# Kernel optimization log

Measured on AMD Instinct MI355X. Metric: run time of the kernel, lower is better.

## Reference

```python
import jax, jax.numpy as jnp
import numpy as np

B, H, W, C = 4, 64, 64, 128
NH, K = 4, 7
HD = C // NH
MLPD = 4 * C
EPS = 1e-5

def _ln(x, g, b):
    m = x.mean(-1, keepdims=True)
    v = ((x - m) ** 2).mean(-1, keepdims=True)
    return (x - m) * jax.lax.rsqrt(v + EPS) * g + b

def setup_inputs() -> dict:
    key = jax.random.key(0)
    ks = jax.random.split(key, 10)
    rn = lambda k, s: jax.random.normal(k, s, dtype=jnp.float32) * 0.02
    return {
        'query': jax.random.normal(ks[0], (B, H, W, C), dtype=jnp.float32),
        'key_value': jax.random.normal(ks[1], (B, H, W, C), dtype=jnp.float32),
        'g1': jnp.ones((C,), jnp.float32), 'b1': jnp.zeros((C,), jnp.float32),
        'g2': jnp.ones((C,), jnp.float32), 'b2': jnp.zeros((C,), jnp.float32),
        'g3': jnp.ones((C,), jnp.float32), 'b3': jnp.zeros((C,), jnp.float32),
        'Wq': rn(ks[2], (C, C)), 'bq': jnp.zeros((C,), jnp.float32),
        'Wkv': rn(ks[3], (C, 2 * C)), 'bkv': jnp.zeros((2 * C,), jnp.float32),
        'Wp': rn(ks[4], (C, C)), 'bp': jnp.zeros((C,), jnp.float32),
        'rpb': rn(ks[5], (NH, 2 * K - 1, 2 * K - 1)),
        'W1': rn(ks[6], (C, MLPD)), 'bm1': jnp.zeros((MLPD,), jnp.float32),
        'W2': rn(ks[7], (MLPD, C)), 'bm2': jnp.zeros((C,), jnp.float32),
    }

def _nat(qn, kvn, Wq, bq, Wkv, bkv, Wp, bp, rpb):
    # NATTEN-style 2D neighborhood attention (clamped KxK window at borders)
    q = (qn @ Wq + bq).reshape(B, H, W, NH, HD) * (HD ** -0.5)
    kv = (kvn @ Wkv + bkv).reshape(B, H, W, 2, NH, HD)
    k, v = kv[..., 0, :, :], kv[..., 1, :, :]
    ii = jnp.clip(jnp.arange(H) - K // 2, 0, H - K)[:, None] + jnp.arange(K)  # [H,K]
    jj = jnp.clip(jnp.arange(W) - K // 2, 0, W - K)[:, None] + jnp.arange(K)  # [W,K]
    def gather(t):  # [B,H,W,NH,HD] -> [B,H,W,NH,K*K,HD]
        t = jnp.take(t, ii, axis=1)   # [B,H,K,W,NH,HD]
        t = jnp.take(t, jj, axis=3)   # [B,H,K,W,K,NH,HD]
        return t.transpose(0, 1, 3, 5, 2, 4, 6).reshape(B, H, W, NH, K * K, HD)
    kn, vn = gather(k), gather(v)
    scores = jnp.einsum('bijhd,bijhnd->bijhn', q, kn)  # [B,H,W,NH,K*K]
    # relative positional bias: offsets in [-(K-1), K-1] -> index into 2K-1 table
    ri = ii - jnp.arange(H)[:, None] + (K - 1)  # [H,K]
    rj = jj - jnp.arange(W)[:, None] + (K - 1)  # [W,K]
    bias = rpb[:, ri]                   # [NH,H,K,2K-1]
    bias = jnp.take(bias, rj, axis=3)   # [NH,H,K,W,K]
    bias = bias.transpose(1, 3, 0, 2, 4).reshape(H, W, NH, K * K)
    attn = jax.nn.softmax(scores + bias[None], axis=-1)
    out = jnp.einsum('bijhn,bijhnd->bijhd', attn, vn).reshape(B, H, W, C)
    return out @ Wp + bp

def reference(query, key_value, g1, b1, g2, b2, g3, b3, Wq, bq, Wkv, bkv, Wp, bp, rpb, W1, bm1, W2, bm2):
    shortcut = key_value
    qn = _ln(query, g1, b1)
    kvn = _ln(key_value, g2, b2)
    x = shortcut + _nat(qn, kvn, Wq, bq, Wkv, bkv, Wp, bp, rpb)
    h = _ln(x, g3, b3)
    h = jax.nn.gelu(h @ W1 + bm1, approximate=False) @ W2 + bm2
    return x + h
```

## Files before the change

kernel.cpp:

```cpp
#include <hip/hip_runtime.h>
#include <math.h>

#define TOK 16384

typedef __attribute__((ext_vector_type(8))) __bf16 bf16x8;
typedef __attribute__((ext_vector_type(4))) float f32x4;

__device__ inline unsigned short f2bf(float f) {
    union { float f; unsigned int u; } v; v.f = f;
    unsigned int r = v.u + 0x7fffu + ((v.u >> 16) & 1u);
    return (unsigned short)(r >> 16);
}

__device__ inline void ln_body(const float* __restrict__ x, const float* __restrict__ g,
                               const float* __restrict__ b, unsigned short* __restrict__ y,
                               int tok, int lane)
{
    float2 v = ((const float2*)(x + (size_t)tok * 128))[lane];
    float s = v.x + v.y;
#pragma unroll
    for (int m = 32; m >= 1; m >>= 1) s += __shfl_xor(s, m);
    float mean = s * (1.0f / 128.0f);
    float dx = v.x - mean, dy = v.y - mean;
    float vs = dx * dx + dy * dy;
#pragma unroll
    for (int m = 32; m >= 1; m >>= 1) vs += __shfl_xor(vs, m);
    float rs = rsqrtf(vs * (1.0f / 128.0f) + 1e-5f);
    float2 gg = ((const float2*)g)[lane];
    float2 bb = ((const float2*)b)[lane];
    float ox = dx * rs * gg.x + bb.x;
    float oy = dy * rs * gg.y + bb.y;
    unsigned int pk = (unsigned int)f2bf(ox) | ((unsigned int)f2bf(oy) << 16);
    ((unsigned int*)(y + (size_t)tok * 128))[lane] = pk;
}

__global__ __launch_bounds__(256) void prep_kernel(
    const float* __restrict__ query, const float* __restrict__ key_value,
    const float* __restrict__ g1, const float* __restrict__ b1,
    const float* __restrict__ g2, const float* __restrict__ b2,
    const float* __restrict__ Wq, const float* __restrict__ Wkv,
    const float* __restrict__ Wp, const float* __restrict__ W1, const float* __restrict__ W2,
    unsigned short* __restrict__ qnh, unsigned short* __restrict__ kvnh,
    unsigned short* __restrict__ Wt)
{
    int blk = blockIdx.x, tid = threadIdx.x;
    if (blk < 8192) {
        int lane = tid & 63;
        if (blk < 4096) ln_body(query,     g1, b1, qnh,  blk * 4 + (tid >> 6), lane);
        else            ln_body(key_value, g2, b2, kvnh, (blk - 4096) * 4 + (tid >> 6), lane);
        return;
    }
    __shared__ float tile[32][33];
    int t = blk - 8192;
    const float* src; unsigned short* dst; int Kd, Nd, li;
    if      (t < 16)  { src = Wq;  dst = Wt;          Kd = 128; Nd = 128; li = t; }
    else if (t < 48)  { src = Wkv; dst = Wt + 16384;  Kd = 128; Nd = 256; li = t - 16; }
    else if (t < 64)  { src = Wp;  dst = Wt + 49152;  Kd = 128; Nd = 128; li = t - 48; }
    else if (t < 128) { src = W1;  dst = Wt + 65536;  Kd = 128; Nd = 512; li = t - 64; }
    else              { src = W2;  dst = Wt + 131072; Kd = 512; Nd = 128; li = t - 128; }
    int ntc = Nd >> 5;
    int k0 = (li / ntc) * 32, n0 = (li % ntc) * 32;
    int r = tid >> 3, c4 = (tid & 7) * 4;
    float4 v = *(const float4*)(src + (size_t)(k0 + r) * Nd + n0 + c4);
    tile[r][c4 + 0] = v.x; tile[r][c4 + 1] = v.y;
    tile[r][c4 + 2] = v.z; tile[r][c4 + 3] = v.w;
    __syncthreads();
    ushort4 o;
    o.x = f2bf(tile[c4 + 0][r]);
    o.y = f2bf(tile[c4 + 1][r]);
    o.z = f2bf(tile[c4 + 2][r]);
    o.w = f2bf(tile[c4 + 3][r]);
    *(ushort4*)(dst + (size_t)(n0 + r) * Kd + k0 + c4) = o;
}

template<int MODE, int TK>
__global__ __launch_bounds__(256) void gemm_mfma(
    const unsigned short* __restrict__ A, const unsigned short* __restrict__ Wt,
    const float* __restrict__ bias, const float* __restrict__ res,
    float* __restrict__ outF, unsigned short* __restrict__ outH,
    unsigned short* __restrict__ vtg, int N, float scale)
{
    const int wave = threadIdx.x >> 6, lane = threadIdx.x & 63;
    const int wm = wave & 1, wn = wave >> 1;
    const int m0 = blockIdx.x * 64 + wm * 32;
    const int n0 = blockIdx.y * 64 + wn * 32;
    const int lr = lane & 15, lg = lane >> 4;
    f32x4 acc[2][2] = {};
#pragma unroll 8
    for (int k0 = 0; k0 < TK; k0 += 32) {
        bf16x8 a[2], b[2];
#pragma unroll
        for (int mf = 0; mf < 2; ++mf)
            a[mf] = *(const bf16x8*)(A + (size_t)(m0 + mf * 16 + lr) * TK + k0 + lg * 8);
#pragma unroll
        for (int nf = 0; nf < 2; ++nf)
            b[nf] = *(const bf16x8*)(Wt + (size_t)(n0 + nf * 16 + lr) * TK + k0 + lg * 8);
#pragma unroll
        for (int mf = 0; mf < 2; ++mf)
#pragma unroll
            for (int nf = 0; nf < 2; ++nf)
                acc[mf][nf] = __builtin_amdgcn_mfma_f32_16x16x32_bf16(a[mf], b[nf], acc[mf][nf], 0, 0, 0);
    }
#pragma unroll
    for (int nf = 0; nf < 2; ++nf) {
        int gc = n0 + nf * 16 + lr;
        float bs = bias[gc];
        if (MODE == 3 && gc >= 128) {
            int d = gc - 128;
            int hh = d >> 5, dd = d & 31;
#pragma unroll
            for (int mf = 0; mf < 2; ++mf) {
                int gr0 = m0 + mf * 16 + lg * 4;
                int bidx = gr0 >> 12, pos = gr0 & 4095;
                ushort4 pk;
                pk.x = f2bf(acc[mf][nf][0] + bs);
                pk.y = f2bf(acc[mf][nf][1] + bs);
                pk.z = f2bf(acc[mf][nf][2] + bs);
                pk.w = f2bf(acc[mf][nf][3] + bs);
                *(ushort4*)(vtg + ((size_t)((bidx * 4 + hh) * 32 + dd)) * 4096 + pos) = pk;
            }
            continue;
        }
#pragma unroll
        for (int mf = 0; mf < 2; ++mf) {
            int gr0 = m0 + mf * 16 + lg * 4;
#pragma unroll
            for (int r = 0; r < 4; ++r) {
                float v = acc[mf][nf][r] + bs;
                if (MODE == 0) outH[(size_t)(gr0 + r) * N + gc] = f2bf(v * scale);
                if (MODE == 1) { size_t idx = (size_t)(gr0 + r) * N + gc; outF[idx] = v + res[idx]; }
                if (MODE == 2) {
                    float gl = 0.5f * v * (1.0f + erff(v * 0.70710678118654752f));
                    outH[(size_t)(gr0 + r) * N + gc] = f2bf(gl);
                }
                if (MODE == 3) outH[(size_t)(gr0 + r) * 128 + gc] = f2bf(v);
            }
        }
    }
}

__global__ __launch_bounds__(256) void gemm_p_ln(
    const unsigned short* __restrict__ A, const unsigned short* __restrict__ Wt,
    const float* __restrict__ bias, const float* __restrict__ res,
    const float* __restrict__ g, const float* __restrict__ bln,
    float* __restrict__ xb, unsigned short* __restrict__ y)
{
    __shared__ float xs[32][132];
    const int wave = threadIdx.x >> 6, lane = threadIdx.x & 63;
    const int m0 = blockIdx.x * 32;
    const int n0 = wave * 32;
    const int lr = lane & 15, lg = lane >> 4;
    f32x4 acc[2][2] = {};
#pragma unroll
    for (int k0 = 0; k0 < 128; k0 += 32) {
        bf16x8 a[2], b[2];
#pragma unroll
        for (int mf = 0; mf < 2; ++mf)
            a[mf] = *(const bf16x8*)(A + (size_t)(m0 + mf * 16 + lr) * 128 + k0 + lg * 8);
#pragma unroll
        for (int nf = 0; nf < 2; ++nf)
            b[nf] = *(const bf16x8*)(Wt + (size_t)(n0 + nf * 16 + lr) * 128 + k0 + lg * 8);
#pragma unroll
        for (int mf = 0; mf < 2; ++mf)
#pragma unroll
            for (int nf = 0; nf < 2; ++nf)
                acc[mf][nf] = __builtin_amdgcn_mfma_f32_16x16x32_bf16(a[mf], b[nf], acc[mf][nf], 0, 0, 0);
    }
#pragma unroll
    for (int nf = 0; nf < 2; ++nf) {
        int gc = n0 + nf * 16 + lr;
        float bs = bias[gc];
#pragma unroll
        for (int mf = 0; mf < 2; ++mf) {
            int lr0 = mf * 16 + lg * 4;
#pragma unroll
            for (int r = 0; r < 4; ++r) {
                size_t idx = (size_t)(m0 + lr0 + r) * 128 + gc;
                float v = acc[mf][nf][r] + bs + res[idx];
                xb[idx] = v;
                xs[lr0 + r][gc] = v;
            }
        }
    }
    __syncthreads();
    const int r = threadIdx.x >> 3, t8 = threadIdx.x & 7;
    float vals[16];
#pragma unroll
    for (int j = 0; j < 16; ++j) vals[j] = xs[r][t8 * 16 + j];
    float s = 0.0f;
#pragma unroll
    for (int j = 0; j < 16; ++j) s += vals[j];
    s += __shfl_xor(s, 1); s += __shfl_xor(s, 2); s += __shfl_xor(s, 4);
    float mean = s * (1.0f / 128.0f);
    float vv = 0.0f;
#pragma unroll
    for (int j = 0; j < 16; ++j) { float d = vals[j] - mean; vv += d * d; }
    vv += __shfl_xor(vv, 1); vv += __shfl_xor(vv, 2); vv += __shfl_xor(vv, 4);
    float rs = rsqrtf(vv * (1.0f / 128.0f) + 1e-5f);
#pragma unroll
    for (int jj = 0; jj < 4; ++jj) {
        float4 gg = ((const float4*)g)[t8 * 4 + jj];
        float4 bb = ((const float4*)bln)[t8 * 4 + jj];
        ushort4 o;
        o.x = f2bf((vals[jj * 4 + 0] - mean) * rs * gg.x + bb.x);
        o.y = f2bf((vals[jj * 4 + 1] - mean) * rs * gg.y + bb.y);
        o.z = f2bf((vals[jj * 4 + 2] - mean) * rs * gg.z + bb.z);
        o.w = f2bf((vals[jj * 4 + 3] - mean) * rs * gg.w + bb.w);
        *(ushort4*)(y + (size_t)(m0 + r) * 128 + t8 * 16 + jj * 4) = o;
    }
}

__global__ __launch_bounds__(256) void nat_attn(
    const unsigned short* __restrict__ qbh,
    const unsigned short* __restrict__ kbh,
    const unsigned short* __restrict__ vtg,
    const float* __restrict__ rpb,
    unsigned short* __restrict__ out)
{
    __shared__ __align__(16) unsigned short Pbuf[4][16][232];
    __shared__ float rpbs[169];
    const int tid = threadIdx.x;
    const int wave = tid >> 6, lane = tid & 63;
    const int c = lane & 15, lg = lane >> 4;
    const int bid = blockIdx.x;
    const int tile = bid & 63, h = (bid >> 6) & 3, b = bid >> 8;
    const int ti0 = (tile >> 3) * 8, tj0 = (tile & 7) * 8;
    const int hr0 = min(max(ti0 - 3, 0), 50);
    const int hc0 = min(max(tj0 - 3, 0), 50);
    const int bb = b << 12;
    if (tid < 169) rpbs[tid] = rpb[h * 169 + tid];
    __syncthreads();

    const int gi_m = ti0 + wave * 2 + (c >> 3);
    const int gj_m = tj0 + (c & 7);
    const int tq = bb + gi_m * 64 + gj_m;
    bf16x8 qf = *(const bf16x8*)(qbh + (size_t)tq * 128 + h * 32 + lg * 8);

    bf16x8 kf[14];
    const int tk0 = bb + hr0 * 64 + hc0 + c;
#pragma unroll
    for (int kb = 0; kb < 14; ++kb)
        kf[kb] = *(const bf16x8*)(kbh + (size_t)(tk0 + kb * 64) * 128 + h * 32 + lg * 8);

    f32x4 S[14];
#pragma unroll
    for (int kb = 0; kb < 14; ++kb) {
        f32x4 z = {0.0f, 0.0f, 0.0f, 0.0f};
        S[kb] = __builtin_amdgcn_mfma_f32_16x16x32_bf16(qf, kf[kb], z, 0, 0, 0);
    }

    bf16x8 vf[7][2];
    const size_t vbase = (size_t)((b * 4 + h) * 32) * 4096;
#pragma unroll
    for (int ks = 0; ks < 7; ++ks) {
        int p0 = ks * 32 + lg * 8;
        size_t posa = (size_t)(hr0 + (p0 >> 4)) * 64 + hc0 + (p0 & 15);
#pragma unroll
        for (int nb = 0; nb < 2; ++nb)
            vf[ks][nb] = *(const bf16x8*)(vtg + vbase + (size_t)(nb * 16 + c) * 4096 + posa);
    }

#pragma unroll
    for (int i = 0; i < 4; ++i) {
        int m = lg * 4 + i;
        int gi = ti0 + wave * 2 + (m >> 3);
        int gj = tj0 + (m & 7);
        int si = min(max(gi - 3, 0), 57), sj = min(max(gj - 3, 0), 57);
        bool cv = (unsigned)(hc0 + c - sj) < 7u;
        int rjc = min(max(hc0 + c - gj + 6, 0), 12);
        float mxi = -INFINITY;
#pragma unroll
        for (int kb = 0; kb < 14; ++kb) {
            bool rv = (unsigned)(hr0 + kb - si) < 7u;
            int ric = min(max(hr0 + kb - gi + 6, 0), 12);
            float bias = rpbs[rjc + ric * 13];
            float s = (rv && cv) ? S[kb][i] + bias : -1e30f;
            S[kb][i] = s;
            mxi = fmaxf(mxi, s);
        }
        mxi = fmaxf(mxi, __shfl_xor(mxi, 1));
        mxi = fmaxf(mxi, __shfl_xor(mxi, 2));
        mxi = fmaxf(mxi, __shfl_xor(mxi, 4));
        mxi = fmaxf(mxi, __shfl_xor(mxi, 8));
        float smi = 0.0f;
#pragma unroll
        for (int kb = 0; kb < 14; ++kb) {
            float e = expf(S[kb][i] - mxi);
            S[kb][i] = e;
            smi += e;
        }
        smi += __shfl_xor(smi, 1);
        smi += __shfl_xor(smi, 2);
        smi += __shfl_xor(smi, 4);
        smi += __shfl_xor(smi, 8);
        float rinv = 1.0f / smi;
#pragma unroll
        for (int kb = 0; kb < 14; ++kb)
            Pbuf[wave][m][kb * 16 + c] = f2bf(S[kb][i] * rinv);
    }

    f32x4 O[2] = {};
#pragma unroll
    for (int ks = 0; ks < 7; ++ks) {
        bf16x8 pf = *(const bf16x8*)&Pbuf[wave][c][ks * 32 + lg * 8];
#pragma unroll
        for (int nb = 0; nb < 2; ++nb)
            O[nb] = __builtin_amdgcn_mfma_f32_16x16x32_bf16(pf, vf[ks][nb], O[nb], 0, 0, 0);
    }
#pragma unroll
    for (int i = 0; i < 4; ++i) {
        int m = lg * 4 + i;
        int gi = ti0 + wave * 2 + (m >> 3);
        int gj = tj0 + (m & 7);
        size_t t = ((size_t)(bb + gi * 64 + gj)) * 128 + h * 32;
        out[t + c]      = f2bf(O[0][i]);
        out[t + 16 + c] = f2bf(O[1][i]);
    }
}

extern "C" void kernel_launch(void* const* d_in, const int* in_sizes, int n_in,
                              void* d_out, int out_size, void* d_ws, size_t ws_size,
                              hipStream_t stream) {
    const float* query     = (const float*)d_in[0];
    const float* key_value = (const float*)d_in[1];
    const float* g1 = (const float*)d_in[2];
    const float* b1 = (const float*)d_in[3];
    const float* g2 = (const float*)d_in[4];
    const float* b2 = (const float*)d_in[5];
    const float* g3 = (const float*)d_in[6];
    const float* b3 = (const float*)d_in[7];
    const float* Wq  = (const float*)d_in[8];
    const float* bq  = (const float*)d_in[9];
    const float* Wkv = (const float*)d_in[10];
    const float* bkv = (const float*)d_in[11];
    const float* Wp  = (const float*)d_in[12];
    const float* bp  = (const float*)d_in[13];
    const float* rpb = (const float*)d_in[14];
    const float* W1  = (const float*)d_in[15];
    const float* bm1 = (const float*)d_in[16];
    const float* W2  = (const float*)d_in[17];
    const float* bm2 = (const float*)d_in[18];

    char* ws = (char*)d_ws;
    float*          xb   = (float*)(ws + 0);
    unsigned short* bufD = (unsigned short*)(ws + 8388608);
    unsigned short* kvnh = (unsigned short*)(ws + 12582912);
    unsigned short* qbh  = (unsigned short*)(ws + 16777216);
    unsigned short* kbh  = (unsigned short*)(ws + 20971520);
    unsigned short* vtg  = (unsigned short*)(ws + 25165824);
    unsigned short* h1h  = (unsigned short*)(ws + 29360128);
    unsigned short* Wt   = (unsigned short*)(ws + 46137344);
    unsigned short* WtQ  = Wt;
    unsigned short* WtKV = Wt + 16384;
    unsigned short* WtP  = Wt + 49152;
    unsigned short* WtW1 = Wt + 65536;
    unsigned short* WtW2 = Wt + 131072;

    const float qscale = 0.17677669529663687f;

    prep_kernel<<<8384, 256, 0, stream>>>(query, key_value, g1, b1, g2, b2,
                                          Wq, Wkv, Wp, W1, W2, bufD, kvnh, Wt);
    gemm_mfma<0,128><<<dim3(256, 2), 256, 0, stream>>>(bufD, WtQ,  bq,  nullptr, nullptr, qbh, nullptr, 128, qscale);
    gemm_mfma<3,128><<<dim3(256, 4), 256, 0, stream>>>(kvnh, WtKV, bkv, nullptr, nullptr, kbh, vtg,     256, 1.0f);
    nat_attn<<<1024, 256, 0, stream>>>(qbh, kbh, vtg, rpb, bufD);
    gemm_p_ln<<<512, 256, 0, stream>>>(bufD, WtP, bp, key_value, g3, b3, xb, kvnh);
    gemm_mfma<2,128><<<dim3(256, 8), 256, 0, stream>>>(kvnh, WtW1, bm1, nullptr, nullptr, h1h, nullptr, 512, 1.0f);
    gemm_mfma<1,512><<<dim3(256, 2), 256, 0, stream>>>(h1h,  WtW2, bm2, xb, (float*)d_out, nullptr, nullptr, 128, 1.0f);
}
```

Before: 206.3 us.

## Merge Q/KV GEMMs, use single-wave GEMM tiles, stage K/V in LDS for attention

Replaces the separate Q and KV projection launches with one gemm_qkv launch. The GEMMs now use 64-thread single-wave blocks, each computing a 32x64 tile. V is written token-major instead of as a transposed global layout, and nat_attn loads the 14x16 K/V halo once into shared memory, transposing V there, instead of each wave gathering K and V from global memory. This removes redundant global loads across the four waves and one launch, at the cost of more shared memory, extra barriers and possible LDS bank conflicts on the strided V transpose writes.

Result: faster. 181.9 us (-11.8%).

```diff
diff --git a/kernel.cpp b/kernel.cpp
--- a/kernel.cpp
+++ b/kernel.cpp
@@ -4,6 +4,7 @@
 #define TOK 16384
 
 typedef __attribute__((ext_vector_type(8))) __bf16 bf16x8;
+typedef __attribute__((ext_vector_type(4))) __bf16 bf16x4;
 typedef __attribute__((ext_vector_type(4))) float f32x4;
 
 __device__ inline unsigned short f2bf(float f) {
@@ -73,67 +74,100 @@
     *(ushort4*)(dst + (size_t)(n0 + r) * Kd + k0 + c4) = o;
 }
 
-template<int MODE, int TK>
-__global__ __launch_bounds__(256) void gemm_mfma(
-    const unsigned short* __restrict__ A, const unsigned short* __restrict__ Wt,
-    const float* __restrict__ bias, const float* __restrict__ res,
-    float* __restrict__ outF, unsigned short* __restrict__ outH,
-    unsigned short* __restrict__ vtg, int N, float scale)
-{
-    const int wave = threadIdx.x >> 6, lane = threadIdx.x & 63;
-    const int wm = wave & 1, wn = wave >> 1;
-    const int m0 = blockIdx.x * 64 + wm * 32;
-    const int n0 = blockIdx.y * 64 + wn * 32;
+__global__ __launch_bounds__(64) void gemm_qkv(
+    const unsigned short* __restrict__ qnh, const unsigned short* __restrict__ kvnh,
+    const unsigned short* __restrict__ Wt,
+    const float* __restrict__ bq, const float* __restrict__ bkv,
+    unsigned short* __restrict__ qbh, unsigned short* __restrict__ kbh,
+    unsigned short* __restrict__ vbh, float qscale)
+{
+    const int lane = threadIdx.x;
     const int lr = lane & 15, lg = lane >> 4;
-    f32x4 acc[2][2] = {};
-#pragma unroll 8
-    for (int k0 = 0; k0 < TK; k0 += 32) {
-        bf16x8 a[2], b[2];
-#pragma unroll
-        for (int mf = 0; mf < 2; ++mf)
-            a[mf] = *(const bf16x8*)(A + (size_t)(m0 + mf * 16 + lr) * TK + k0 + lg * 8);
-#pragma unroll
-        for (int nf = 0; nf < 2; ++nf)
-            b[nf] = *(const bf16x8*)(Wt + (size_t)(n0 + nf * 16 + lr) * TK + k0 + lg * 8);
-#pragma unroll
-        for (int mf = 0; mf < 2; ++mf)
-#pragma unroll
-            for (int nf = 0; nf < 2; ++nf)
+    const int y = blockIdx.y;
+    const unsigned short* A;
+    const unsigned short* Wb;
+    const float* bias;
+    int n0;
+    if (y < 2) { A = qnh;  Wb = Wt;          bias = bq;  n0 = y * 64; }
+    else       { A = kvnh; Wb = Wt + 16384;  bias = bkv; n0 = (y - 2) * 64; }
+    const int m0 = blockIdx.x * 32;
+    f32x4 acc[2][4] = {};
+#pragma unroll
+    for (int k0 = 0; k0 < 128; k0 += 32) {
+        bf16x8 a[2], b[4];
+#pragma unroll
+        for (int mf = 0; mf < 2; ++mf)
+            a[mf] = *(const bf16x8*)(A + (size_t)(m0 + mf * 16 + lr) * 128 + k0 + lg * 8);
+#pragma unroll
+        for (int nf = 0; nf < 4; ++nf)
+            b[nf] = *(const bf16x8*)(Wb + (size_t)(n0 + nf * 16 + lr) * 128 + k0 + lg * 8);
+#pragma unroll
+        for (int mf = 0; mf < 2; ++mf)
+#pragma unroll
+            for (int nf = 0; nf < 4; ++nf)
                 acc[mf][nf] = __builtin_amdgcn_mfma_f32_16x16x32_bf16(a[mf], b[nf], acc[mf][nf], 0, 0, 0);
     }
 #pragma unroll
-    for (int nf = 0; nf < 2; ++nf) {
+    for (int nf = 0; nf < 4; ++nf) {
         int gc = n0 + nf * 16 + lr;
         float bs = bias[gc];
-        if (MODE == 3 && gc >= 128) {
-            int d = gc - 128;
-            int hh = d >> 5, dd = d & 31;
-#pragma unroll
-            for (int mf = 0; mf < 2; ++mf) {
-                int gr0 = m0 + mf * 16 + lg * 4;
-                int bidx = gr0 >> 12, pos = gr0 & 4095;
-                ushort4 pk;
-                pk.x = f2bf(acc[mf][nf][0] + bs);
-                pk.y = f2bf(acc[mf][nf][1] + bs);
-                pk.z = f2bf(acc[mf][nf][2] + bs);
-                pk.w = f2bf(acc[mf][nf][3] + bs);
-                *(ushort4*)(vtg + ((size_t)((bidx * 4 + hh) * 32 + dd)) * 4096 + pos) = pk;
-            }
-            continue;
-        }
 #pragma unroll
         for (int mf = 0; mf < 2; ++mf) {
             int gr0 = m0 + mf * 16 + lg * 4;
 #pragma unroll
             for (int r = 0; r < 4; ++r) {
                 float v = acc[mf][nf][r] + bs;
-                if (MODE == 0) outH[(size_t)(gr0 + r) * N + gc] = f2bf(v * scale);
-                if (MODE == 1) { size_t idx = (size_t)(gr0 + r) * N + gc; outF[idx] = v + res[idx]; }
+                size_t tok = (size_t)(gr0 + r);
+                if (y < 2)          qbh[tok * 128 + gc] = f2bf(v * qscale);
+                else if (gc < 128)  kbh[tok * 128 + gc] = f2bf(v);
+                else                vbh[tok * 128 + gc - 128] = f2bf(v);
+            }
+        }
+    }
+}
+
+template<int MODE, int TK>
+__global__ __launch_bounds__(64) void gemm_w(
+    const unsigned short* __restrict__ A, const unsigned short* __restrict__ Wb,
+    const float* __restrict__ bias, const float* __restrict__ res,
+    float* __restrict__ outF, unsigned short* __restrict__ outH, int N)
+{
+    const int lane = threadIdx.x;
+    const int lr = lane & 15, lg = lane >> 4;
+    const int m0 = blockIdx.x * 32;
+    const int n0 = blockIdx.y * 64;
+    f32x4 acc[2][4] = {};
+#pragma unroll 4
+    for (int k0 = 0; k0 < TK; k0 += 32) {
+        bf16x8 a[2], b[4];
+#pragma unroll
+        for (int mf = 0; mf < 2; ++mf)
+            a[mf] = *(const bf16x8*)(A + (size_t)(m0 + mf * 16 + lr) * TK + k0 + lg * 8);
+#pragma unroll
+        for (int nf = 0; nf < 4; ++nf)
+            b[nf] = *(const bf16x8*)(Wb + (size_t)(n0 + nf * 16 + lr) * TK + k0 + lg * 8);
+#pragma unroll
+        for (int mf = 0; mf < 2; ++mf)
+#pragma unroll
+            for (int nf = 0; nf < 4; ++nf)
+                acc[mf][nf] = __builtin_amdgcn_mfma_f32_16x16x32_bf16(a[mf], b[nf], acc[mf][nf], 0, 0, 0);
+    }
+#pragma unroll
+    for (int nf = 0; nf < 4; ++nf) {
+        int gc = n0 + nf * 16 + lr;
+        float bs = bias[gc];
+#pragma unroll
+        for (int mf = 0; mf < 2; ++mf) {
+            int gr0 = m0 + mf * 16 + lg * 4;
+#pragma unroll
+            for (int r = 0; r < 4; ++r) {
+                float v = acc[mf][nf][r] + bs;
+                size_t idx = (size_t)(gr0 + r) * N + gc;
+                if (MODE == 1) outF[idx] = v + res[idx];
                 if (MODE == 2) {
                     float gl = 0.5f * v * (1.0f + erff(v * 0.70710678118654752f));
-                    outH[(size_t)(gr0 + r) * N + gc] = f2bf(gl);
+                    outH[idx] = f2bf(gl);
                 }
-                if (MODE == 3) outH[(size_t)(gr0 + r) * 128 + gc] = f2bf(v);
             }
         }
     }
@@ -213,11 +247,12 @@
 __global__ __launch_bounds__(256) void nat_attn(
     const unsigned short* __restrict__ qbh,
     const unsigned short* __restrict__ kbh,
-    const unsigned short* __restrict__ vtg,
+    const unsigned short* __restrict__ vbh,
     const float* __restrict__ rpb,
     unsigned short* __restrict__ out)
 {
-    __shared__ __align__(16) unsigned short Pbuf[4][16][232];
+    __shared__ unsigned short KP[14848];
+    __shared__ unsigned short Vsm[32 * 232];
     __shared__ float rpbs[169];
     const int tid = threadIdx.x;
     const int wave = tid >> 6, lane = tid & 63;
@@ -228,37 +263,36 @@
     const int hr0 = min(max(ti0 - 3, 0), 50);
     const int hc0 = min(max(tj0 - 3, 0), 50);
     const int bb = b << 12;
+
     if (tid < 169) rpbs[tid] = rpb[h * 169 + tid];
-    __syncthreads();
+
+    for (int u = tid; u < 896; u += 256) {
+        int tok = u >> 2, chunk = u & 3;
+        int tr = tok >> 4, tc = tok & 15;
+        size_t src = (size_t)(bb + (hr0 + tr) * 64 + hc0 + tc) * 128 + h * 32 + chunk * 8;
+        int4 kw = *(const int4*)(kbh + src);
+        *(int4*)&KP[tok * 40 + chunk * 8] = kw;
+        int4 vw = *(const int4*)(vbh + src);
+        const unsigned short* v8 = (const unsigned short*)&vw;
+#pragma unroll
+        for (int k = 0; k < 8; ++k)
+            Vsm[(chunk * 8 + k) * 232 + tok] = v8[k];
+    }
 
     const int gi_m = ti0 + wave * 2 + (c >> 3);
     const int gj_m = tj0 + (c & 7);
     const int tq = bb + gi_m * 64 + gj_m;
     bf16x8 qf = *(const bf16x8*)(qbh + (size_t)tq * 128 + h * 32 + lg * 8);
-
-    bf16x8 kf[14];
-    const int tk0 = bb + hr0 * 64 + hc0 + c;
-#pragma unroll
-    for (int kb = 0; kb < 14; ++kb)
-        kf[kb] = *(const bf16x8*)(kbh + (size_t)(tk0 + kb * 64) * 128 + h * 32 + lg * 8);
+    __syncthreads();
 
     f32x4 S[14];
 #pragma unroll
     for (int kb = 0; kb < 14; ++kb) {
+        bf16x8 kf = *(const bf16x8*)&KP[(kb * 16 + c) * 40 + lg * 8];
         f32x4 z = {0.0f, 0.0f, 0.0f, 0.0f};
-        S[kb] = __builtin_amdgcn_mfma_f32_16x16x32_bf16(qf, kf[kb], z, 0, 0, 0);
-    }
-
-    bf16x8 vf[7][2];
-    const size_t vbase = (size_t)((b * 4 + h) * 32) * 4096;
-#pragma unroll
-    for (int ks = 0; ks < 7; ++ks) {
-        int p0 = ks * 32 + lg * 8;
-        size_t posa = (size_t)(hr0 + (p0 >> 4)) * 64 + hc0 + (p0 & 15);
-#pragma unroll
-        for (int nb = 0; nb < 2; ++nb)
-            vf[ks][nb] = *(const bf16x8*)(vtg + vbase + (size_t)(nb * 16 + c) * 4096 + posa);
-    }
+        S[kb] = __builtin_amdgcn_mfma_f32_16x16x32_bf16(qf, kf, z, 0, 0, 0);
+    }
+    __syncthreads();
 
 #pragma unroll
     for (int i = 0; i < 4; ++i) {
@@ -296,16 +330,24 @@
         float rinv = 1.0f / smi;
 #pragma unroll
         for (int kb = 0; kb < 14; ++kb)
-            Pbuf[wave][m][kb * 16 + c] = f2bf(S[kb][i] * rinv);
+            KP[(wave * 16 + m) * 232 + kb * 16 + c] = f2bf(S[kb][i] * rinv);
     }
 
     f32x4 O[2] = {};
 #pragma unroll
     for (int ks = 0; ks < 7; ++ks) {
-        bf16x8 pf = *(const bf16x8*)&Pbuf[wave][c][ks * 32 + lg * 8];
-#pragma unroll
-        for (int nb = 0; nb < 2; ++nb)
-            O[nb] = __builtin_amdgcn_mfma_f32_16x16x32_bf16(pf, vf[ks][nb], O[nb], 0, 0, 0);
+        int po = (wave * 16 + c) * 232 + ks * 32 + lg * 8;
+        bf16x4 plo = *(const bf16x4*)&KP[po];
+        bf16x4 phi = *(const bf16x4*)&KP[po + 4];
+        bf16x8 pf = __builtin_shufflevector(plo, phi, 0, 1, 2, 3, 4, 5, 6, 7);
+#pragma unroll
+        for (int nb = 0; nb < 2; ++nb) {
+            int vo = (nb * 16 + c) * 232 + ks * 32 + lg * 8;
+            bf16x4 vlo = *(const bf16x4*)&Vsm[vo];
+            bf16x4 vhi = *(const bf16x4*)&Vsm[vo + 4];
+            bf16x8 vf = __builtin_shufflevector(vlo, vhi, 0, 1, 2, 3, 4, 5, 6, 7);
+            O[nb] = __builtin_amdgcn_mfma_f32_16x16x32_bf16(pf, vf, O[nb], 0, 0, 0);
+        }
     }
 #pragma unroll
     for (int i = 0; i < 4; ++i) {
@@ -347,11 +389,9 @@
     unsigned short* kvnh = (unsigned short*)(ws + 12582912);
     unsigned short* qbh  = (unsigned short*)(ws + 16777216);
     unsigned short* kbh  = (unsigned short*)(ws + 20971520);
-    unsigned short* vtg  = (unsigned short*)(ws + 25165824);
+    unsigned short* vbh  = (unsigned short*)(ws + 25165824);
     unsigned short* h1h  = (unsigned short*)(ws + 29360128);
     unsigned short* Wt   = (unsigned short*)(ws + 46137344);
-    unsigned short* WtQ  = Wt;
-    unsigned short* WtKV = Wt + 16384;
     unsigned short* WtP  = Wt + 49152;
     unsigned short* WtW1 = Wt + 65536;
     unsigned short* WtW2 = Wt + 131072;
@@ -360,10 +400,9 @@
 
     prep_kernel<<<8384, 256, 0, stream>>>(query, key_value, g1, b1, g2, b2,
                                           Wq, Wkv, Wp, W1, W2, bufD, kvnh, Wt);
-    gemm_mfma<0,128><<<dim3(256, 2), 256, 0, stream>>>(bufD, WtQ,  bq,  nullptr, nullptr, qbh, nullptr, 128, qscale);
-    gemm_mfma<3,128><<<dim3(256, 4), 256, 0, stream>>>(kvnh, WtKV, bkv, nullptr, nullptr, kbh, vtg,     256, 1.0f);
-    nat_attn<<<1024, 256, 0, stream>>>(qbh, kbh, vtg, rpb, bufD);
+    gemm_qkv<<<dim3(512, 6), 64, 0, stream>>>(bufD, kvnh, Wt, bq, bkv, qbh, kbh, vbh, qscale);
+    nat_attn<<<1024, 256, 0, stream>>>(qbh, kbh, vbh, rpb, bufD);
     gemm_p_ln<<<512, 256, 0, stream>>>(bufD, WtP, bp, key_value, g3, b3, xb, kvnh);
-    gemm_mfma<2,128><<<dim3(256, 8), 256, 0, stream>>>(kvnh, WtW1, bm1, nullptr, nullptr, h1h, nullptr, 512, 1.0f);
-    gemm_mfma<1,512><<<dim3(256, 2), 256, 0, stream>>>(h1h,  WtW2, bm2, xb, (float*)d_out, nullptr, nullptr, 128, 1.0f);
-}
+    gemm_w<2, 128><<<dim3(512, 8), 64, 0, stream>>>(kvnh, WtW1, bm1, nullptr, nullptr, h1h, 512);
+    gemm_w<1, 512><<<dim3(512, 2), 64, 0, stream>>>(h1h,  WtW2, bm2, xb, (float*)d_out, nullptr, 128);
+}
```

## Fuse QKV projection into attention and fuse proj+LN+MLP into one tail kernel

Applied to the files above, without the earlier changes.

Q/K/V projections are now computed inside the neighborhood-attention kernel for each tile's halo. K, Q and transposed V are staged in shared memory instead of being written to and reread from global buffers. The output projection, residual, LayerNorm, both MLP GEMMs with GELU and the final residual are fused into one kernel per 32-token block, with intermediates kept in LDS. This removes five launches and several global round trips, but the attention kernel recomputes K/V for overlapping halos (about 3.5x redundant KV work), and the tail kernel uses large LDS, which may limit occupancy.

Result: faster. 198.8 us (-3.7%).

```diff
diff --git a/kernel.cpp b/kernel.cpp
--- a/kernel.cpp
+++ b/kernel.cpp
@@ -10,6 +10,9 @@
     union { float f; unsigned int u; } v; v.f = f;
     unsigned int r = v.u + 0x7fffu + ((v.u >> 16) & 1u);
     return (unsigned short)(r >> 16);
+}
+__device__ inline float gelu_exact(float v) {
+    return 0.5f * v * (1.0f + erff(v * 0.70710678118654752f));
 }
 
 __device__ inline void ln_body(const float* __restrict__ x, const float* __restrict__ g,
@@ -73,155 +76,24 @@
     *(ushort4*)(dst + (size_t)(n0 + r) * Kd + k0 + c4) = o;
 }
 
-template<int MODE, int TK>
-__global__ __launch_bounds__(256) void gemm_mfma(
-    const unsigned short* __restrict__ A, const unsigned short* __restrict__ Wt,
-    const float* __restrict__ bias, const float* __restrict__ res,
-    float* __restrict__ outF, unsigned short* __restrict__ outH,
-    unsigned short* __restrict__ vtg, int N, float scale)
+__global__ __launch_bounds__(256) void natqkv(
+    const unsigned short* __restrict__ qnh,
+    const unsigned short* __restrict__ kvnh,
+    const unsigned short* __restrict__ Wt,
+    const float* __restrict__ bq, const float* __restrict__ bkv,
+    const float* __restrict__ rpb,
+    unsigned short* __restrict__ out,
+    float qscale)
 {
-    const int wave = threadIdx.x >> 6, lane = threadIdx.x & 63;
-    const int wm = wave & 1, wn = wave >> 1;
-    const int m0 = blockIdx.x * 64 + wm * 32;
-    const int n0 = blockIdx.y * 64 + wn * 32;
-    const int lr = lane & 15, lg = lane >> 4;
-    f32x4 acc[2][2] = {};
-#pragma unroll 8
-    for (int k0 = 0; k0 < TK; k0 += 32) {
-        bf16x8 a[2], b[2];
-#pragma unroll
-        for (int mf = 0; mf < 2; ++mf)
-            a[mf] = *(const bf16x8*)(A + (size_t)(m0 + mf * 16 + lr) * TK + k0 + lg * 8);
-#pragma unroll
-        for (int nf = 0; nf < 2; ++nf)
-            b[nf] = *(const bf16x8*)(Wt + (size_t)(n0 + nf * 16 + lr) * TK + k0 + lg * 8);
-#pragma unroll
-        for (int mf = 0; mf < 2; ++mf)
-#pragma unroll
-            for (int nf = 0; nf < 2; ++nf)
-                acc[mf][nf] = __builtin_amdgcn_mfma_f32_16x16x32_bf16(a[mf], b[nf], acc[mf][nf], 0, 0, 0);
-    }
-#pragma unroll
-    for (int nf = 0; nf < 2; ++nf) {
-        int gc = n0 + nf * 16 + lr;
-        float bs = bias[gc];
-        if (MODE == 3 && gc >= 128) {
-            int d = gc - 128;
-            int hh = d >> 5, dd = d & 31;
-#pragma unroll
-            for (int mf = 0; mf < 2; ++mf) {
-                int gr0 = m0 + mf * 16 + lg * 4;
-                int bidx = gr0 >> 12, pos = gr0 & 4095;
-                ushort4 pk;
-                pk.x = f2bf(acc[mf][nf][0] + bs);
-                pk.y = f2bf(acc[mf][nf][1] + bs);
-                pk.z = f2bf(acc[mf][nf][2] + bs);
-                pk.w = f2bf(acc[mf][nf][3] + bs);
-                *(ushort4*)(vtg + ((size_t)((bidx * 4 + hh) * 32 + dd)) * 4096 + pos) = pk;
-            }
-            continue;
-        }
-#pragma unroll
-        for (int mf = 0; mf < 2; ++mf) {
-            int gr0 = m0 + mf * 16 + lg * 4;
-#pragma unroll
-            for (int r = 0; r < 4; ++r) {
-                float v = acc[mf][nf][r] + bs;
-                if (MODE == 0) outH[(size_t)(gr0 + r) * N + gc] = f2bf(v * scale);
-                if (MODE == 1) { size_t idx = (size_t)(gr0 + r) * N + gc; outF[idx] = v + res[idx]; }
-                if (MODE == 2) {
-                    float gl = 0.5f * v * (1.0f + erff(v * 0.70710678118654752f));
-                    outH[(size_t)(gr0 + r) * N + gc] = f2bf(gl);
-                }
-                if (MODE == 3) outH[(size_t)(gr0 + r) * 128 + gc] = f2bf(v);
-            }
-        }
-    }
-}
-
-__global__ __launch_bounds__(256) void gemm_p_ln(
-    const unsigned short* __restrict__ A, const unsigned short* __restrict__ Wt,
-    const float* __restrict__ bias, const float* __restrict__ res,
-    const float* __restrict__ g, const float* __restrict__ bln,
-    float* __restrict__ xb, unsigned short* __restrict__ y)
-{
-    __shared__ float xs[32][132];
-    const int wave = threadIdx.x >> 6, lane = threadIdx.x & 63;
-    const int m0 = blockIdx.x * 32;
-    const int n0 = wave * 32;
-    const int lr = lane & 15, lg = lane >> 4;
-    f32x4 acc[2][2] = {};
-#pragma unroll
-    for (int k0 = 0; k0 < 128; k0 += 32) {
-        bf16x8 a[2], b[2];
-#pragma unroll
-        for (int mf = 0; mf < 2; ++mf)
-            a[mf] = *(const bf16x8*)(A + (size_t)(m0 + mf * 16 + lr) * 128 + k0 + lg * 8);
-#pragma unroll
-        for (int nf = 0; nf < 2; ++nf)
-            b[nf] = *(const bf16x8*)(Wt + (size_t)(n0 + nf * 16 + lr) * 128 + k0 + lg * 8);
-#pragma unroll
-        for (int mf = 0; mf < 2; ++mf)
-#pragma unroll
-            for (int nf = 0; nf < 2; ++nf)
-                acc[mf][nf] = __builtin_amdgcn_mfma_f32_16x16x32_bf16(a[mf], b[nf], acc[mf][nf], 0, 0, 0);
-    }
-#pragma unroll
-    for (int nf = 0; nf < 2; ++nf) {
-        int gc = n0 + nf * 16 + lr;
-        float bs = bias[gc];
-#pragma unroll
-        for (int mf = 0; mf < 2; ++mf) {
-            int lr0 = mf * 16 + lg * 4;
-#pragma unroll
-            for (int r = 0; r < 4; ++r) {
-                size_t idx = (size_t)(m0 + lr0 + r) * 128 + gc;
-                float v = acc[mf][nf][r] + bs + res[idx];
-                xb[idx] = v;
-                xs[lr0 + r][gc] = v;
-            }
-        }
-    }
-    __syncthreads();
-    const int r = threadIdx.x >> 3, t8 = threadIdx.x & 7;
-    float vals[16];
-#pragma unroll
-    for (int j = 0; j < 16; ++j) vals[j] = xs[r][t8 * 16 + j];
-    float s = 0.0f;
-#pragma unroll
-    for (int j = 0; j < 16; ++j) s += vals[j];
-    s += __shfl_xor(s, 1); s += __shfl_xor(s, 2); s += __shfl_xor(s, 4);
-    float mean = s * (1.0f / 128.0f);
-    float vv = 0.0f;
-#pragma unroll
-    for (int j = 0; j < 16; ++j) { float d = vals[j] - mean; vv += d * d; }
-    vv += __shfl_xor(vv, 1); vv += __shfl_xor(vv, 2); vv += __shfl_xor(vv, 4);
-    float rs = rsqrtf(vv * (1.0f / 128.0f) + 1e-5f);
-#pragma unroll
-    for (int jj = 0; jj < 4; ++jj) {
-        float4 gg = ((const float4*)g)[t8 * 4 + jj];
-        float4 bb = ((const float4*)bln)[t8 * 4 + jj];
-        ushort4 o;
-        o.x = f2bf((vals[jj * 4 + 0] - mean) * rs * gg.x + bb.x);
-        o.y = f2bf((vals[jj * 4 + 1] - mean) * rs * gg.y + bb.y);
-        o.z = f2bf((vals[jj * 4 + 2] - mean) * rs * gg.z + bb.z);
-        o.w = f2bf((vals[jj * 4 + 3] - mean) * rs * gg.w + bb.w);
-        *(ushort4*)(y + (size_t)(m0 + r) * 128 + t8 * 16 + jj * 4) = o;
-    }
-}
-
-__global__ __launch_bounds__(256) void nat_attn(
-    const unsigned short* __restrict__ qbh,
-    const unsigned short* __restrict__ kbh,
-    const unsigned short* __restrict__ vtg,
-    const float* __restrict__ rpb,
-    unsigned short* __restrict__ out)
-{
-    __shared__ __align__(16) unsigned short Pbuf[4][16][232];
+    __shared__ __align__(16) unsigned short shm[22272];
     __shared__ float rpbs[169];
+    unsigned short* kS = shm;
+    unsigned short* qS = shm + 8960;
+    unsigned short* P  = shm;
+    unsigned short* vT = shm + 14848;
     const int tid = threadIdx.x;
     const int wave = tid >> 6, lane = tid & 63;
-    const int c = lane & 15, lg = lane >> 4;
+    const int lr = lane & 15, lg = lane >> 4;
     const int bid = blockIdx.x;
     const int tile = bid & 63, h = (bid >> 6) & 3, b = bid >> 8;
     const int ti0 = (tile >> 3) * 8, tj0 = (tile & 7) * 8;
@@ -229,36 +101,81 @@
     const int hc0 = min(max(tj0 - 3, 0), 50);
     const int bb = b << 12;
     if (tid < 169) rpbs[tid] = rpb[h * 169 + tid];
-    __syncthreads();
-
-    const int gi_m = ti0 + wave * 2 + (c >> 3);
-    const int gj_m = tj0 + (c & 7);
-    const int tq = bb + gi_m * 64 + gj_m;
-    bf16x8 qf = *(const bf16x8*)(qbh + (size_t)tq * 128 + h * 32 + lg * 8);
-
-    bf16x8 kf[14];
-    const int tk0 = bb + hr0 * 64 + hc0 + c;
-#pragma unroll
-    for (int kb = 0; kb < 14; ++kb)
-        kf[kb] = *(const bf16x8*)(kbh + (size_t)(tk0 + kb * 64) * 128 + h * 32 + lg * 8);
-
+
+    const unsigned short* WtKV = Wt + 16384;
+
+    {
+        const bool vjob = wave >= 2;
+        const int n0 = vjob ? 128 + h * 32 + (wave - 2) * 16 : h * 32 + wave * 16;
+        const unsigned short* wrow = WtKV + (size_t)(n0 + lr) * 128;
+        bf16x8 wf[4];
+#pragma unroll
+        for (int kk = 0; kk < 4; ++kk) wf[kk] = *(const bf16x8*)(wrow + kk * 32 + lg * 8);
+#pragma unroll
+        for (int rt = 0; rt < 14; ++rt) {
+            int tok = bb + (hr0 + rt) * 64 + hc0 + lr;
+            const unsigned short* asrc = kvnh + (size_t)tok * 128;
+            f32x4 acc = {0.f, 0.f, 0.f, 0.f};
+#pragma unroll
+            for (int kk = 0; kk < 4; ++kk) {
+                bf16x8 xf = *(const bf16x8*)(asrc + kk * 32 + lg * 8);
+                acc = vjob ? __builtin_amdgcn_mfma_f32_16x16x32_bf16(xf, wf[kk], acc, 0, 0, 0)
+                           : __builtin_amdgcn_mfma_f32_16x16x32_bf16(wf[kk], xf, acc, 0, 0, 0);
+            }
+            if (!vjob) {
+                int chb = wave * 16 + lg * 4;
+                float4 bs = *(const float4*)(bkv + h * 32 + chb);
+                ushort4 pk;
+                pk.x = f2bf(acc[0] + bs.x); pk.y = f2bf(acc[1] + bs.y);
+                pk.z = f2bf(acc[2] + bs.z); pk.w = f2bf(acc[3] + bs.w);
+                *(ushort4*)&kS[(rt * 16 + lr) * 40 + chb] = pk;
+            } else {
+                int chl = (wave - 2) * 16 + lr;
+                float bs = bkv[128 + h * 32 + chl];
+                ushort4 pk;
+                pk.x = f2bf(acc[0] + bs); pk.y = f2bf(acc[1] + bs);
+                pk.z = f2bf(acc[2] + bs); pk.w = f2bf(acc[3] + bs);
+                *(ushort4*)&vT[chl * 232 + rt * 16 + lg * 4] = pk;
+            }
+        }
+    }
+    {
+        const int colt = wave & 1;
+        const unsigned short* wrow = Wt + (size_t)(h * 32 + colt * 16 + lr) * 128;
+        bf16x8 wf[4];
+#pragma unroll
+        for (int kk = 0; kk < 4; ++kk) wf[kk] = *(const bf16x8*)(wrow + kk * 32 + lg * 8);
+#pragma unroll
+        for (int tt = 0; tt < 2; ++tt) {
+            int qrt = (wave >> 1) + tt * 2;
+            int qi = qrt * 16 + lr;
+            int tok = bb + (ti0 + (qi >> 3)) * 64 + tj0 + (qi & 7);
+            const unsigned short* asrc = qnh + (size_t)tok * 128;
+            f32x4 acc = {0.f, 0.f, 0.f, 0.f};
+#pragma unroll
+            for (int kk = 0; kk < 4; ++kk) {
+                bf16x8 xf = *(const bf16x8*)(asrc + kk * 32 + lg * 8);
+                acc = __builtin_amdgcn_mfma_f32_16x16x32_bf16(wf[kk], xf, acc, 0, 0, 0);
+            }
+            int chb = colt * 16 + lg * 4;
+            float4 bs = *(const float4*)(bq + h * 32 + chb);
+            ushort4 pk;
+            pk.x = f2bf((acc[0] + bs.x) * qscale); pk.y = f2bf((acc[1] + bs.y) * qscale);
+            pk.z = f2bf((acc[2] + bs.z) * qscale); pk.w = f2bf((acc[3] + bs.w) * qscale);
+            *(ushort4*)&qS[(qrt * 16 + lr) * 40 + chb] = pk;
+        }
+    }
+    __syncthreads();
+
+    bf16x8 qf = *(const bf16x8*)&qS[(wave * 16 + lr) * 40 + lg * 8];
     f32x4 S[14];
 #pragma unroll
     for (int kb = 0; kb < 14; ++kb) {
-        f32x4 z = {0.0f, 0.0f, 0.0f, 0.0f};
-        S[kb] = __builtin_amdgcn_mfma_f32_16x16x32_bf16(qf, kf[kb], z, 0, 0, 0);
-    }
-
-    bf16x8 vf[7][2];
-    const size_t vbase = (size_t)((b * 4 + h) * 32) * 4096;
-#pragma unroll
-    for (int ks = 0; ks < 7; ++ks) {
-        int p0 = ks * 32 + lg * 8;
-        size_t posa = (size_t)(hr0 + (p0 >> 4)) * 64 + hc0 + (p0 & 15);
-#pragma unroll
-        for (int nb = 0; nb < 2; ++nb)
-            vf[ks][nb] = *(const bf16x8*)(vtg + vbase + (size_t)(nb * 16 + c) * 4096 + posa);
-    }
+        bf16x8 kf = *(const bf16x8*)&kS[(kb * 16 + lr) * 40 + lg * 8];
+        f32x4 z = {0.f, 0.f, 0.f, 0.f};
+        S[kb] = __builtin_amdgcn_mfma_f32_16x16x32_bf16(qf, kf, z, 0, 0, 0);
+    }
+    __syncthreads();
 
 #pragma unroll
     for (int i = 0; i < 4; ++i) {
@@ -266,8 +183,8 @@
         int gi = ti0 + wave * 2 + (m >> 3);
         int gj = tj0 + (m & 7);
         int si = min(max(gi - 3, 0), 57), sj = min(max(gj - 3, 0), 57);
-        bool cv = (unsigned)(hc0 + c - sj) < 7u;
-        int rjc = min(max(hc0 + c - gj + 6, 0), 12);
+        bool cv = (unsigned)(hc0 + lr - sj) < 7u;
+        int rjc = min(max(hc0 + lr - gj + 6, 0), 12);
         float mxi = -INFINITY;
 #pragma unroll
         for (int kb = 0; kb < 14; ++kb) {
@@ -296,16 +213,18 @@
         float rinv = 1.0f / smi;
 #pragma unroll
         for (int kb = 0; kb < 14; ++kb)
-            Pbuf[wave][m][kb * 16 + c] = f2bf(S[kb][i] * rinv);
+            P[(wave * 16 + m) * 232 + kb * 16 + lr] = f2bf(S[kb][i] * rinv);
     }
 
     f32x4 O[2] = {};
 #pragma unroll
     for (int ks = 0; ks < 7; ++ks) {
-        bf16x8 pf = *(const bf16x8*)&Pbuf[wave][c][ks * 32 + lg * 8];
-#pragma unroll
-        for (int nb = 0; nb < 2; ++nb)
-            O[nb] = __builtin_amdgcn_mfma_f32_16x16x32_bf16(pf, vf[ks][nb], O[nb], 0, 0, 0);
+        bf16x8 pf = *(const bf16x8*)&P[(wave * 16 + lr) * 232 + ks * 32 + lg * 8];
+#pragma unroll
+        for (int nb = 0; nb < 2; ++nb) {
+            bf16x8 vf = *(const bf16x8*)&vT[(nb * 16 + lr) * 232 + ks * 32 + lg * 8];
+            O[nb] = __builtin_amdgcn_mfma_f32_16x16x32_bf16(pf, vf, O[nb], 0, 0, 0);
+        }
     }
 #pragma unroll
     for (int i = 0; i < 4; ++i) {
@@ -313,8 +232,120 @@
         int gi = ti0 + wave * 2 + (m >> 3);
         int gj = tj0 + (m & 7);
         size_t t = ((size_t)(bb + gi * 64 + gj)) * 128 + h * 32;
-        out[t + c]      = f2bf(O[0][i]);
-        out[t + 16 + c] = f2bf(O[1][i]);
+        out[t + lr]      = f2bf(O[0][i]);
+        out[t + 16 + lr] = f2bf(O[1][i]);
+    }
+}
+
+__global__ __launch_bounds__(256) void tail_kernel(
+    const unsigned short* __restrict__ attnh,
+    const unsigned short* __restrict__ WtP,
+    const unsigned short* __restrict__ W1t,
+    const unsigned short* __restrict__ W2t,
+    const float* __restrict__ bp, const float* __restrict__ bm1, const float* __restrict__ bm2,
+    const float* __restrict__ resk,
+    const float* __restrict__ g3, const float* __restrict__ b3,
+    float* __restrict__ dout)
+{
+    __shared__ float xs[32][132];
+    __shared__ __align__(16) unsigned short xnS[32 * 136];
+    __shared__ __align__(16) unsigned short hS[32 * 520];
+    const int tid = threadIdx.x;
+    const int wave = tid >> 6, lane = tid & 63;
+    const int lr = lane & 15, lg = lane >> 4;
+    const int m0 = blockIdx.x * 32;
+
+#pragma unroll
+    for (int t = 0; t < 4; ++t) {
+        int j = t * 4 + wave;
+        int rowt = j >> 3, colt = j & 7;
+        int tok = m0 + rowt * 16 + lr;
+        f32x4 acc = {0.f, 0.f, 0.f, 0.f};
+#pragma unroll
+        for (int kk = 0; kk < 4; ++kk) {
+            bf16x8 af = *(const bf16x8*)(attnh + (size_t)tok * 128 + kk * 32 + lg * 8);
+            bf16x8 wf = *(const bf16x8*)(WtP + (size_t)(colt * 16 + lr) * 128 + kk * 32 + lg * 8);
+            acc = __builtin_amdgcn_mfma_f32_16x16x32_bf16(af, wf, acc, 0, 0, 0);
+        }
+        int gc = colt * 16 + lr;
+        float bs = bp[gc];
+#pragma unroll
+        for (int r = 0; r < 4; ++r) {
+            int row = rowt * 16 + lg * 4 + r;
+            xs[row][gc] = acc[r] + bs + resk[(size_t)(m0 + row) * 128 + gc];
+        }
+    }
+    __syncthreads();
+
+    {
+        const int r = tid >> 3, t8 = tid & 7;
+        float vals[16];
+#pragma unroll
+        for (int jj = 0; jj < 16; ++jj) vals[jj] = xs[r][t8 * 16 + jj];
+        float s = 0.0f;
+#pragma unroll
+        for (int jj = 0; jj < 16; ++jj) s += vals[jj];
+        s += __shfl_xor(s, 1); s += __shfl_xor(s, 2); s += __shfl_xor(s, 4);
+        float mean = s * (1.0f / 128.0f);
+        float vv = 0.0f;
+#pragma unroll
+        for (int jj = 0; jj < 16; ++jj) { float d = vals[jj] - mean; vv += d * d; }
+        vv += __shfl_xor(vv, 1); vv += __shfl_xor(vv, 2); vv += __shfl_xor(vv, 4);
+        float rs = rsqrtf(vv * (1.0f / 128.0f) + 1e-5f);
+#pragma unroll
+        for (int jj = 0; jj < 4; ++jj) {
+            float4 gg = ((const float4*)g3)[t8 * 4 + jj];
+            float4 bb = ((const float4*)b3)[t8 * 4 + jj];
+            ushort4 o;
+            o.x = f2bf((vals[jj * 4 + 0] - mean) * rs * gg.x + bb.x);
+            o.y = f2bf((vals[jj * 4 + 1] - mean) * rs * gg.y + bb.y);
+            o.z = f2bf((vals[jj * 4 + 2] - mean) * rs * gg.z + bb.z);
+            o.w = f2bf((vals[jj * 4 + 3] - mean) * rs * gg.w + bb.w);
+            *(ushort4*)&xnS[r * 136 + t8 * 16 + jj * 4] = o;
+        }
+    }
+    __syncthreads();
+
+#pragma unroll
+    for (int t = 0; t < 16; ++t) {
+        int j = t * 4 + wave;
+        int rowt = j >> 5, colt = j & 31;
+        f32x4 acc = {0.f, 0.f, 0.f, 0.f};
+#pragma unroll
+        for (int kk = 0; kk < 4; ++kk) {
+            bf16x8 wf = *(const bf16x8*)(W1t + (size_t)(colt * 16 + lr) * 128 + kk * 32 + lg * 8);
+            bf16x8 xf = *(const bf16x8*)&xnS[(rowt * 16 + lr) * 136 + kk * 32 + lg * 8];
+            acc = __builtin_amdgcn_mfma_f32_16x16x32_bf16(wf, xf, acc, 0, 0, 0);
+        }
+        int chb = colt * 16 + lg * 4;
+        float4 bs = *(const float4*)(bm1 + chb);
+        ushort4 pk;
+        pk.x = f2bf(gelu_exact(acc[0] + bs.x));
+        pk.y = f2bf(gelu_exact(acc[1] + bs.y));
+        pk.z = f2bf(gelu_exact(acc[2] + bs.z));
+        pk.w = f2bf(gelu_exact(acc[3] + bs.w));
+        *(ushort4*)&hS[(rowt * 16 + lr) * 520 + chb] = pk;
+    }
+    __syncthreads();
+
+#pragma unroll
+    for (int t = 0; t < 4; ++t) {
+        int j = t * 4 + wave;
+        int rowt = j >> 3, colt = j & 7;
+        f32x4 acc = {0.f, 0.f, 0.f, 0.f};
+#pragma unroll
+        for (int kk = 0; kk < 16; ++kk) {
+            bf16x8 hf = *(const bf16x8*)&hS[(rowt * 16 + lr) * 520 + kk * 32 + lg * 8];
+            bf16x8 wf = *(const bf16x8*)(W2t + (size_t)(colt * 16 + lr) * 512 + kk * 32 + lg * 8);
+            acc = __builtin_amdgcn_mfma_f32_16x16x32_bf16(hf, wf, acc, 0, 0, 0);
+        }
+        int gc = colt * 16 + lr;
+        float bs = bm2[gc];
+#pragma unroll
+        for (int r = 0; r < 4; ++r) {
+            int row = rowt * 16 + lg * 4 + r;
+            dout[(size_t)(m0 + row) * 128 + gc] = acc[r] + bs + xs[row][gc];
+        }
     }
 }
 
@@ -342,28 +373,16 @@
     const float* bm2 = (const float*)d_in[18];
 
     char* ws = (char*)d_ws;
-    float*          xb   = (float*)(ws + 0);
-    unsigned short* bufD = (unsigned short*)(ws + 8388608);
-    unsigned short* kvnh = (unsigned short*)(ws + 12582912);
-    unsigned short* qbh  = (unsigned short*)(ws + 16777216);
-    unsigned short* kbh  = (unsigned short*)(ws + 20971520);
-    unsigned short* vtg  = (unsigned short*)(ws + 25165824);
-    unsigned short* h1h  = (unsigned short*)(ws + 29360128);
-    unsigned short* Wt   = (unsigned short*)(ws + 46137344);
-    unsigned short* WtQ  = Wt;
-    unsigned short* WtKV = Wt + 16384;
-    unsigned short* WtP  = Wt + 49152;
-    unsigned short* WtW1 = Wt + 65536;
-    unsigned short* WtW2 = Wt + 131072;
+    unsigned short* qnh   = (unsigned short*)(ws + 0);
+    unsigned short* kvnh  = (unsigned short*)(ws + 4194304);
+    unsigned short* attnh = (unsigned short*)(ws + 8388608);
+    unsigned short* Wt    = (unsigned short*)(ws + 12582912);
 
     const float qscale = 0.17677669529663687f;
 
     prep_kernel<<<8384, 256, 0, stream>>>(query, key_value, g1, b1, g2, b2,
-                                          Wq, Wkv, Wp, W1, W2, bufD, kvnh, Wt);
-    gemm_mfma<0,128><<<dim3(256, 2), 256, 0, stream>>>(bufD, WtQ,  bq,  nullptr, nullptr, qbh, nullptr, 128, qscale);
-    gemm_mfma<3,128><<<dim3(256, 4), 256, 0, stream>>>(kvnh, WtKV, bkv, nullptr, nullptr, kbh, vtg,     256, 1.0f);
-    nat_attn<<<1024, 256, 0, stream>>>(qbh, kbh, vtg, rpb, bufD);
-    gemm_p_ln<<<512, 256, 0, stream>>>(bufD, WtP, bp, key_value, g3, b3, xb, kvnh);
-    gemm_mfma<2,128><<<dim3(256, 8), 256, 0, stream>>>(kvnh, WtW1, bm1, nullptr, nullptr, h1h, nullptr, 512, 1.0f);
-    gemm_mfma<1,512><<<dim3(256, 2), 256, 0, stream>>>(h1h,  WtW2, bm2, xb, (float*)d_out, nullptr, nullptr, 128, 1.0f);
-}
+                                          Wq, Wkv, Wp, W1, W2, qnh, kvnh, Wt);
+    natqkv<<<1024, 256, 0, stream>>>(qnh, kvnh, Wt, bq, bkv, rpb, attnh, qscale);
+    tail_kernel<<<512, 256, 0, stream>>>(attnh, Wt + 49152, Wt + 65536, Wt + 131072,
+                                         bp, bm1, bm2, key_value, g3, b3, (float*)d_out);
+}
```
